# Kernel tuning notes

Measured on AMD Instinct MI355X. Metric: run time of the kernel, lower is better.

The kernel has to match this reference:

```python
import jax, jax.numpy as jnp
import numpy as np
from jax import lax

N_POINTS = 400000
WIDTH = 64  # 3 xyz + 61 payload features
STRIDE = 400


def setup_inputs() -> dict:
    key = jax.random.key(0)
    feats = jax.random.normal(key, (N_POINTS, WIDTH), dtype=jnp.float32)
    return {"feats": feats}


def _furthest_point_sampling(p, m):
    """Iterative FPS over p: [N, 3], returning m int32 indices.

    Mirrors pointops.furthestsampling: seed with index 0, maintain running
    min squared distance to the sampled set, pick argmax each step.
    """
    n = p.shape[0]
    init_dists = jnp.full((n,), 1e10, dtype=p.dtype)

    def step(carry, _):
        dists, last = carry
        # squared distance from every point to the most recently sampled point
        d = jnp.sum(jnp.square(p - p[last]), axis=-1)  # [N]
        dists = jnp.minimum(dists, d)
        nxt = jnp.argmax(dists).astype(jnp.int32)
        return (dists, nxt), nxt

    (_, _), rest = lax.scan(step, (init_dists, jnp.int32(0)), None, length=m - 1)
    return jnp.concatenate([jnp.zeros((1,), dtype=jnp.int32), rest])


def reference(feats):
    p = feats[:, :3]  # xyz coordinates; feats[:, 3:] are unused payload
    n = feats.shape[0]
    m = n // STRIDE  # n_o = [N // stride] for the single batch
    idx = _furthest_point_sampling(p, m)
    return idx
```

## Files before the change

### kernel.cpp

```cpp
#include <hip/hip_runtime.h>
#include <stdint.h>

#define N_POINTS   400000
#define WIDTH      64
#define M_SAMPLES  1000
#define NBLK       32
#define NTHR       512
#define NWAVE      (NTHR / 64)
#define NTOT       (NBLK * NTHR)
#define PPT        25
#define TAIL_GID   (N_POINTS - (PPT - 1) * NTOT)
#define EPAD       8
#define SLOT_WORDS ((M_SAMPLES - 1) * NBLK * EPAD)


__global__ void fps_init(unsigned long long* slot, int* out) {
    int t = blockIdx.x * blockDim.x + threadIdx.x;
    if (t < SLOT_WORDS) slot[t] = 0ull;
    if (t == 0) out[0] = 0;
}

template <int STAGES, int SRCLANE>
__device__ inline unsigned long long wave_scan_max_u64(unsigned long long key) {
    unsigned int lo = (unsigned int)key;
    unsigned int hi = (unsigned int)(key >> 32);
#define FPS_DPP_STAGE(CTRL)                                                     \
    {                                                                           \
        unsigned int nlo = (unsigned int)__builtin_amdgcn_update_dpp(           \
            (int)lo, (int)lo, CTRL, 0xf, 0xf, false);                           \
        unsigned int nhi = (unsigned int)__builtin_amdgcn_update_dpp(           \
            (int)hi, (int)hi, CTRL, 0xf, 0xf, false);                           \
        unsigned long long cand = ((unsigned long long)nhi << 32) | nlo;        \
        unsigned long long cur  = ((unsigned long long)hi  << 32) | lo;         \
        if (cand > cur) { lo = nlo; hi = nhi; }                                 \
    }
    if constexpr (STAGES > 0) FPS_DPP_STAGE(0x111)
    if constexpr (STAGES > 1) FPS_DPP_STAGE(0x112)
    if constexpr (STAGES > 2) FPS_DPP_STAGE(0x114)
    if constexpr (STAGES > 3) FPS_DPP_STAGE(0x118)
    if constexpr (STAGES > 4) FPS_DPP_STAGE(0x142)
    if constexpr (STAGES > 5) FPS_DPP_STAGE(0x143)
#undef FPS_DPP_STAGE
    unsigned int rlo = (unsigned int)__builtin_amdgcn_readlane((int)lo, SRCLANE);
    unsigned int rhi = (unsigned int)__builtin_amdgcn_readlane((int)hi, SRCLANE);
    return ((unsigned long long)rhi << 32) | rlo;
}

__global__ __launch_bounds__(NTHR)
void fps_main(const float* __restrict__ feats, int* __restrict__ out,
              unsigned long long* __restrict__ slot)
{
    const int tid  = threadIdx.x;
    const int bid  = blockIdx.x;
    const int lane = tid & 63;
    const int wid  = tid >> 6;
    const int gid  = bid * NTHR + tid;

    float px[PPT], py[PPT], pz[PPT], dd[PPT];
#pragma unroll
    for (int k = 0; k < PPT; k++) {
        int j = gid + k * NTOT;
        if (j < N_POINTS) {
            float4 v = *reinterpret_cast<const float4*>(feats + (size_t)j * WIDTH);
            px[k] = v.x; py[k] = v.y; pz[k] = v.z;
        } else {
            px[k] = 0.f; py[k] = 0.f; pz[k] = 0.f;
        }
        dd[k] = 1e10f;
    }

    __shared__ unsigned long long s_wmax[NWAVE];
    __shared__ float s_qx, s_qy, s_qz;

    float qx = feats[0];
    float qy = feats[1];
    float qz = feats[2];

    for (int i = 1; i < M_SAMPLES; i++) {
        float bd = -1.0f;
        unsigned int bj = 0;
#pragma unroll
        for (int k = 0; k < PPT; k++) {
            int j = gid + k * NTOT;
            float dx = __fsub_rn(px[k], qx);
            float dy = __fsub_rn(py[k], qy);
            float dz = __fsub_rn(pz[k], qz);
            float d  = __fadd_rn(__fadd_rn(__fmul_rn(dx, dx), __fmul_rn(dy, dy)),
                                 __fmul_rn(dz, dz));
            float nd = fminf(dd[k], d);
            dd[k] = nd;
            bool upd = (nd > bd);
            if (k == PPT - 1) upd = upd && (gid < TAIL_GID);
            bd = upd ? nd : bd;
            bj = upd ? (unsigned int)j : bj;
        }
        unsigned long long key =
            ((unsigned long long)__float_as_uint(bd) << 32) |
            (unsigned long long)(unsigned int)(N_POINTS - bj);

        unsigned long long wmax = wave_scan_max_u64<6, 63>(key);
        if (lane == 0) s_wmax[wid] = wmax;
        __syncthreads();

        unsigned long long* cur = slot + (size_t)(i - 1) * NBLK * EPAD;
        if (wid == 0) {
            unsigned long long bk = (lane < NWAVE) ? s_wmax[lane] : 0ull;
            unsigned long long blockmax = wave_scan_max_u64<3, 7>(bk);
            if (lane == 0)
                __hip_atomic_store(&cur[(size_t)bid * EPAD], blockmax,
                                   __ATOMIC_RELAXED, __HIP_MEMORY_SCOPE_AGENT);

            unsigned long long e = 0ull;
            if (lane < NBLK) {
                do {
                    e = __hip_atomic_load(&cur[(size_t)lane * EPAD],
                                          __ATOMIC_RELAXED,
                                          __HIP_MEMORY_SCOPE_AGENT);
                } while (e == 0ull);
            }

            unsigned int widx = 0;
            float4 pv = make_float4(0.f, 0.f, 0.f, 0.f);
            if (lane < NBLK) {
                widx = N_POINTS - (unsigned int)(e & 0xffffffffull);
                pv = *reinterpret_cast<const float4*>(feats + (size_t)widx * WIDTH);
            }

            unsigned long long win =
                wave_scan_max_u64<5, 31>((lane < NBLK) ? e : 0ull);

            if (lane < NBLK && e == win) {
                s_qx = pv.x; s_qy = pv.y; s_qz = pv.z;
                if (bid == 0) out[i] = (int)widx;
            }
        }
        __syncthreads();
        qx = s_qx; qy = s_qy; qz = s_qz;
    }
}

extern "C" void kernel_launch(void* const* d_in, const int* in_sizes, int n_in,
                              void* d_out, int out_size, void* d_ws, size_t ws_size,
                              hipStream_t stream) {
    const float* feats = (const float*)d_in[0];
    int* out = (int*)d_out;
    unsigned long long* slot = (unsigned long long*)d_ws;

    fps_init<<<(SLOT_WORDS + 255) / 256, 256, 0, stream>>>(slot, out);
    fps_main<<<NBLK, NTHR, 0, stream>>>(feats, out, slot);
}
```

Before: 2.703 ms.

## Double block count and use tagged ring buffer for inter-block argmax exchange

Raises the grid from 32 to 64 blocks, which halves the points each thread holds in registers, and lets a full wave of lanes each poll one block's slot. The per-iteration slot array is replaced by a 128-entry ring buffer, and each slot value carries an 8-bit iteration tag packed into the low key bits, so readers wait for the matching tag instead of for a nonzero value. This cuts per-step distance work and shrinks the zero-initialised workspace, at the cost of a wider grid-wide barrier each iteration. It also relies on the ring depth being enough that no block overwrites a slot another block has not yet read.

```diff
diff --git a/kernel.cpp b/kernel.cpp
--- a/kernel.cpp
+++ b/kernel.cpp
@@ -4,14 +4,15 @@
 #define N_POINTS   400000
 #define WIDTH      64
 #define M_SAMPLES  1000
-#define NBLK       32
+#define NBLK       64
 #define NTHR       512
 #define NWAVE      (NTHR / 64)
 #define NTOT       (NBLK * NTHR)
-#define PPT        25
+#define PPT        13
 #define TAIL_GID   (N_POINTS - (PPT - 1) * NTOT)
 #define EPAD       8
-#define SLOT_WORDS ((M_SAMPLES - 1) * NBLK * EPAD)
+#define NREG       128
+#define SLOT_WORDS (NREG * NBLK * EPAD)
 
 
 __global__ void fps_init(unsigned long long* slot, int* out) {
@@ -77,6 +78,9 @@
     float qz = feats[2];
 
     for (int i = 1; i < M_SAMPLES; i++) {
+        const unsigned long long tg = (unsigned long long)(i & 255);
+        unsigned long long* cur = slot + (size_t)((i - 1) & (NREG - 1)) * NBLK * EPAD;
+
         float bd = -1.0f;
         unsigned int bj = 0;
 #pragma unroll
@@ -96,13 +100,13 @@
         }
         unsigned long long key =
             ((unsigned long long)__float_as_uint(bd) << 32) |
-            (unsigned long long)(unsigned int)(N_POINTS - bj);
+            (tg << 19) |
+            (unsigned long long)(N_POINTS - bj);
 
         unsigned long long wmax = wave_scan_max_u64<6, 63>(key);
         if (lane == 0) s_wmax[wid] = wmax;
         __syncthreads();
 
-        unsigned long long* cur = slot + (size_t)(i - 1) * NBLK * EPAD;
         if (wid == 0) {
             unsigned long long bk = (lane < NWAVE) ? s_wmax[lane] : 0ull;
             unsigned long long blockmax = wave_scan_max_u64<3, 7>(bk);
@@ -110,26 +114,18 @@
                 __hip_atomic_store(&cur[(size_t)bid * EPAD], blockmax,
                                    __ATOMIC_RELAXED, __HIP_MEMORY_SCOPE_AGENT);
 
-            unsigned long long e = 0ull;
-            if (lane < NBLK) {
-                do {
-                    e = __hip_atomic_load(&cur[(size_t)lane * EPAD],
-                                          __ATOMIC_RELAXED,
-                                          __HIP_MEMORY_SCOPE_AGENT);
-                } while (e == 0ull);
-            }
+            unsigned long long e;
+            do {
+                e = __hip_atomic_load(&cur[(size_t)lane * EPAD],
+                                      __ATOMIC_RELAXED, __HIP_MEMORY_SCOPE_AGENT);
+            } while (((e >> 19) & 255ull) != tg);
 
-            unsigned int widx = 0;
-            float4 pv = make_float4(0.f, 0.f, 0.f, 0.f);
-            if (lane < NBLK) {
-                widx = N_POINTS - (unsigned int)(e & 0xffffffffull);
-                pv = *reinterpret_cast<const float4*>(feats + (size_t)widx * WIDTH);
-            }
+            unsigned int widx = N_POINTS - (unsigned int)(e & 0x7FFFFull);
+            float4 pv = *reinterpret_cast<const float4*>(feats + (size_t)widx * WIDTH);
 
-            unsigned long long win =
-                wave_scan_max_u64<5, 31>((lane < NBLK) ? e : 0ull);
+            unsigned long long win = wave_scan_max_u64<6, 63>(e);
 
-            if (lane < NBLK && e == win) {
+            if (e == win) {
                 s_qx = pv.x; s_qy = pv.y; s_qz = pv.z;
                 if (bid == 0) out[i] = (int)widx;
             }
```

New measurement: 2.241 ms. -17.1%, faster.
